# Kernel optimization log

Measured on AMD Instinct MI355X. Metric: run time of the kernel, lower is better.

Reference implementation:

```python
import jax, jax.numpy as jnp
import numpy as np

HIDDEN = 1024
NUM_HEADS = 16
HEAD_DIM = HIDDEN // NUM_HEADS


def setup_inputs() -> dict:
    key = jax.random.key(0)
    ks = jax.random.split(key, 9)
    s = 0.02
    return {
        "x": jax.random.normal(ks[0], (2, 2048, HIDDEN), dtype=jnp.float32),
        "wq": jax.random.normal(ks[1], (HIDDEN, HIDDEN), dtype=jnp.float32) * s,
        "bq": jnp.zeros((HIDDEN,), dtype=jnp.float32),
        "wk": jax.random.normal(ks[2], (HIDDEN, HIDDEN), dtype=jnp.float32) * s,
        "bk": jnp.zeros((HIDDEN,), dtype=jnp.float32),
        "wv": jax.random.normal(ks[3], (HIDDEN, HIDDEN), dtype=jnp.float32) * s,
        "bv": jnp.zeros((HIDDEN,), dtype=jnp.float32),
        "wo": jax.random.normal(ks[4], (HIDDEN, HIDDEN), dtype=jnp.float32) * s,
        "bo": jnp.zeros((HIDDEN,), dtype=jnp.float32),
    }


def reference(x, wq, bq, wk, bk, wv, bv, wo, bo):
    B, S, H = x.shape
    # torch nn.Linear: y = x @ W.T + b
    q = x @ wq.T + bq
    k = x @ wk.T + bk
    v = x @ wv.T + bv
    # [B, S, nH, dH] -> [B, nH, S, dH]
    q = q.reshape(B, S, NUM_HEADS, HEAD_DIM).transpose(0, 2, 1, 3)
    k = k.reshape(B, S, NUM_HEADS, HEAD_DIM).transpose(0, 2, 1, 3)
    v = v.reshape(B, S, NUM_HEADS, HEAD_DIM).transpose(0, 2, 1, 3)
    scores = jnp.einsum("bhqd,bhkd->bhqk", q, k)
    probs = jax.nn.softmax(scores / jnp.sqrt(jnp.float32(HEAD_DIM)), axis=-1)
    context = jnp.einsum("bhqk,bhkd->bhqd", probs, v)
    context = context.transpose(0, 2, 1, 3).reshape(B, S, H)
    return context @ wo.T + bo
```

## Files before the change

### kernel.cpp

```cpp
#include <hip/hip_runtime.h>
#include <hip/hip_bf16.h>
#include <math.h>

#define HID   1024
#define NHEAD 16
#define DHEAD 64
#define BATCH 2
#define SEQ   2048
#define TOK   (BATCH*SEQ)

#define LOG2E_8 0.18033688011112042f

typedef float f32x4  __attribute__((ext_vector_type(4)));
typedef short short8 __attribute__((ext_vector_type(8)));

__device__ __forceinline__ unsigned short f2bf(float f) {
    unsigned int u = __float_as_uint(f);
    u += 0x7FFFu + ((u >> 16) & 1u);
    return (unsigned short)(u >> 16);
}

__device__ __forceinline__ unsigned pk2(float lo, float hi) {
    union { __hip_bfloat162 h; unsigned u; } cv;
    cv.h = __float22bfloat162_rn(make_float2(lo, hi));
    return cv.u;
}

__device__ __forceinline__ float fexp2(float x) {
#if __has_builtin(__builtin_amdgcn_exp2f)
    return __builtin_amdgcn_exp2f(x);
#else
    return __expf(x * 0.6931471805599453f);
#endif
}

__device__ __forceinline__ void gll16(const unsigned short* g, unsigned short* l) {
    __builtin_amdgcn_global_load_lds(
        (const __attribute__((address_space(1))) void*)g,
        (__attribute__((address_space(3))) void*)l, 16, 0, 0);
}

__global__ __launch_bounds__(256) void cvt_bf16(const float* __restrict__ in,
                                                unsigned short* __restrict__ out, int n8) {
    int i = blockIdx.x * 256 + threadIdx.x;
    if (i >= n8) return;
    const float4* p = (const float4*)in;
    float4 a = p[2*i], b = p[2*i+1];
    uint4 r;
    r.x = pk2(a.x, a.y); r.y = pk2(a.z, a.w);
    r.z = pk2(b.x, b.y); r.w = pk2(b.z, b.w);
    ((uint4*)out)[i] = r;
}

__global__ __launch_bounds__(256) void cvt_bf16_w4(
    const float* __restrict__ i0, const float* __restrict__ i1,
    const float* __restrict__ i2, const float* __restrict__ i3,
    unsigned short* __restrict__ o0, unsigned short* __restrict__ o1,
    unsigned short* __restrict__ o2, unsigned short* __restrict__ o3, int n8) {
    int i = blockIdx.x * 256 + threadIdx.x;
    if (i >= n8) return;
    int z = blockIdx.y;
    const float* in = (z==0)?i0:((z==1)?i1:((z==2)?i2:i3));
    unsigned short* out = (z==0)?o0:((z==1)?o1:((z==2)?o2:o3));
    const float s = (z == 0) ? LOG2E_8 : 1.0f;
    const float4* p = (const float4*)in;
    float4 a = p[2*i], b = p[2*i+1];
    uint4 r;
    r.x = pk2(a.x*s, a.y*s); r.y = pk2(a.z*s, a.w*s);
    r.z = pk2(b.x*s, b.y*s); r.w = pk2(b.z*s, b.w*s);
    ((uint4*)out)[i] = r;
}

template<int BM, int BN, int NZ, bool OUTF32, int MINW>
__global__ __launch_bounds__(256, MINW) void gemm_t(
    const unsigned short* __restrict__ A,
    const unsigned short* __restrict__ W0, const unsigned short* __restrict__ W1,
    const unsigned short* __restrict__ W2,
    const float* __restrict__ b0, const float* __restrict__ b1, const float* __restrict__ b2,
    void* __restrict__ C0, void* __restrict__ C1, void* __restrict__ C2,
    int M, int N, int K)
{
    constexpr int MT = BM/32;
    constexpr int NT = BN/32;
    constexpr int AG = BM/64;
    constexpr int WG = BN/64;

    __shared__ unsigned short As[BM*32];
    __shared__ unsigned short Ws[BN*32];

    const unsigned short* W = W0; const float* bias = b0; void* C = C0;
    int z = 0;
    if (NZ > 1) {
        z = blockIdx.z;
        W    = (z==0) ? W0 : ((z==1) ? W1 : W2);
        bias = (z==0) ? b0 : ((z==1) ? b1 : b2);
        C    = (z==0) ? C0 : ((z==1) ? C1 : C2);
    }
    const int tid  = threadIdx.x;
    const int l15  = tid & 15, quad = (tid >> 4) & 3, w = tid >> 6;
    const int wm   = (w >> 1) * (BM/2), wn = (w & 1) * (BN/2);
    const int m0   = blockIdx.y * BM, n0 = blockIdx.x * BN;

    const int lane = tid & 63;
    const int grow = lane >> 2;
    const int gchk = (lane & 3) ^ (grow & 3);

    const unsigned short* pA[AG]; unsigned short* lA[AG];
    const unsigned short* pW[WG]; unsigned short* lW[WG];
    #pragma unroll
    for (int i = 0; i < AG; ++i) {
        const int r = w*(BM/4) + i*16;
        pA[i] = A + (size_t)(m0 + r + grow) * K + gchk*8;
        lA[i] = &As[r * 32];
    }
    #pragma unroll
    for (int i = 0; i < WG; ++i) {
        const int r = w*(BN/4) + i*16;
        pW[i] = W + (size_t)(n0 + r + grow) * K + gchk*8;
        lW[i] = &Ws[r * 32];
    }

    f32x4 acc[MT][NT] = {};

    for (int k0 = 0; k0 < K; k0 += 32) {
        #pragma unroll
        for (int i = 0; i < AG; ++i) { gll16(pA[i], lA[i]); pA[i] += 32; }
        #pragma unroll
        for (int i = 0; i < WG; ++i) { gll16(pW[i], lW[i]); pW[i] += 32; }
        __syncthreads();

        const int co = (quad ^ (l15 & 3)) * 8;
        short8 af[MT], bfv[NT];
        #pragma unroll
        for (int mi = 0; mi < MT; ++mi) af[mi]  = *(const short8*)&As[(wm + mi*16 + l15)*32 + co];
        #pragma unroll
        for (int ni = 0; ni < NT; ++ni) bfv[ni] = *(const short8*)&Ws[(wn + ni*16 + l15)*32 + co];
        #pragma unroll
        for (int mi = 0; mi < MT; ++mi)
            #pragma unroll
            for (int ni = 0; ni < NT; ++ni)
                acc[mi][ni] = __builtin_amdgcn_mfma_f32_16x16x32_bf16(af[mi], bfv[ni], acc[mi][ni], 0, 0, 0);
        __syncthreads();
    }

    const float bsc = (NZ == 3 && z == 0) ? LOG2E_8 : 1.0f;
    float bv[NT];
    #pragma unroll
    for (int ni = 0; ni < NT; ++ni) bv[ni] = bias[n0 + wn + ni*16 + l15] * bsc;

    if (NZ == 3 && z == 2) {
        #pragma unroll
        for (int mi = 0; mi < MT; ++mi)
            #pragma unroll
            for (int ni = 0; ni < NT; ++ni) {
                const int row0 = m0 + wm + mi*16 + quad*4;
                const int col  = n0 + wn + ni*16 + l15;
                const int hh = col >> 6, dd = col & 63;
                const int bb = row0 >> 11, ss = row0 & 2047;
                ushort4 r4;
                r4.x = f2bf(acc[mi][ni][0] + bv[ni]);
                r4.y = f2bf(acc[mi][ni][1] + bv[ni]);
                r4.z = f2bf(acc[mi][ni][2] + bv[ni]);
                r4.w = f2bf(acc[mi][ni][3] + bv[ni]);
                *(ushort4*)((unsigned short*)C + ((size_t)(bb*NHEAD + hh)*DHEAD + dd)*SEQ + ss) = r4;
            }
    } else {
        #pragma unroll
        for (int mi = 0; mi < MT; ++mi)
            #pragma unroll
            for (int ni = 0; ni < NT; ++ni)
                #pragma unroll
                for (int r = 0; r < 4; ++r) {
                    const int row = m0 + wm + mi*16 + quad*4 + r;
                    const int col = n0 + wn + ni*16 + l15;
                    const float val = acc[mi][ni][r] + bv[ni];
                    if (OUTF32) ((float*)C)[(size_t)row*N + col] = val;
                    else ((unsigned short*)C)[(size_t)row*N + col] = f2bf(val);
                }
    }
}

__global__ __launch_bounds__(256, 2) void attn_v5(
    const unsigned short* __restrict__ Qg, const unsigned short* __restrict__ Kg,
    const unsigned short* __restrict__ vT,
    unsigned short* __restrict__ pO0, unsigned short* __restrict__ pO1,
    float* __restrict__ pl)
{
    __shared__ unsigned short Ks[2][64][64];
    __shared__ unsigned short VT[2][64][64];
    __shared__ unsigned short PTs[4*64*64];

    const int tid  = threadIdx.x;
    const int l15  = tid & 15, quad = (tid >> 4) & 3, w = tid >> 6;
    const int z    = blockIdx.z;
    const int b    = z & 1, half = z >> 1;
    const int h    = blockIdx.y;
    const int q0   = blockIdx.x * 256;
    const size_t rowbase = (size_t)b * SEQ;
    const int    cbase   = h * DHEAD;
    const size_t vbase   = (size_t)(b*NHEAD + h) * DHEAD * SEQ;
    const int    keybase = half * (SEQ/2);

    {
        const unsigned short* src = Qg + (rowbase + q0 + tid) * HID + cbase;
        #pragma unroll
        for (int j = 0; j < 8; ++j)
            *(uint4*)&PTs[tid*64 + ((j ^ (tid & 7)) * 8)] = *(const uint4*)(src + j*8);
    }
    short8 qa[4][2];
    #pragma unroll
    for (int nq = 0; nq < 4; ++nq)
        #pragma unroll
        for (int s2 = 0; s2 < 2; ++s2)
            qa[nq][s2] = *(const short8*)&PTs[(w*64 + nq*16 + l15)*64 + (((s2*4 + quad) ^ (l15 & 7)) * 8)];

    const int sr = tid >> 2, sc = (tid & 3) * 16;
    const int c0 = (sc >> 3) ^ (sr & 7);
    const int c1 = ((sc >> 3) + 1) ^ (sr & 7);
    {
        const unsigned short* ks = Kg + (rowbase + keybase + sr) * HID + cbase + sc;
        const unsigned short* vs = vT + vbase + (size_t)sr * SEQ + keybase + sc;
        *(uint4*)&Ks[0][sr][c0*8] = *(const uint4*)ks;
        *(uint4*)&Ks[0][sr][c1*8] = *(const uint4*)(ks + 8);
        *(uint4*)&VT[0][sr][c0*8] = *(const uint4*)vs;
        *(uint4*)&VT[0][sr][c1*8] = *(const uint4*)(vs + 8);
    }

    f32x4 o[4][4] = {};
    float lsum[4] = {0.f, 0.f, 0.f, 0.f};
    unsigned short* myPT = &PTs[w*64*64];

    for (int kt = 0; kt < SEQ/2/64; ++kt) {
        const int buf = kt & 1;
        __syncthreads();

        uint4 kr0, kr1, vr0, vr1;
        const bool pre = (kt + 1 < SEQ/2/64);
        if (pre) {
            const unsigned short* ks = Kg + (rowbase + keybase + (kt+1)*64 + sr) * HID + cbase + sc;
            const unsigned short* vs = vT + vbase + (size_t)sr * SEQ + keybase + (kt+1)*64 + sc;
            kr0 = *(const uint4*)ks; kr1 = *(const uint4*)(ks + 8);
            vr0 = *(const uint4*)vs; vr1 = *(const uint4*)(vs + 8);
        }

        f32x4 s[4][4] = {};
        #pragma unroll
        for (int s2 = 0; s2 < 2; ++s2) {
            short8 kfr[4];
            #pragma unroll
            for (int mi = 0; mi < 4; ++mi)
                kfr[mi] = *(const short8*)&Ks[buf][mi*16 + l15][((s2*4 + quad) ^ (l15 & 7)) * 8];
            #pragma unroll
            for (int mi = 0; mi < 4; ++mi)
                #pragma unroll
                for (int nq = 0; nq < 4; ++nq)
                    s[mi][nq] = __builtin_amdgcn_mfma_f32_16x16x32_bf16(kfr[mi], qa[nq][s2], s[mi][nq], 0, 0, 0);
        }

        #pragma unroll
        for (int mi = 0; mi < 4; ++mi)
            #pragma unroll
            for (int nq = 0; nq < 4; ++nq) {
                const float p0 = fexp2(s[mi][nq][0]);
                const float p1 = fexp2(s[mi][nq][1]);
                const float p2 = fexp2(s[mi][nq][2]);
                const float p3 = fexp2(s[mi][nq][3]);
                lsum[nq] += (p0 + p1) + (p2 + p3);
                uint2 u; u.x = pk2(p0, p1); u.y = pk2(p2, p3);
                const int off = (((2*mi + (quad >> 1)) ^ (l15 & 7)) * 8) + (quad & 1) * 4;
                *(uint2*)&myPT[(nq*16 + l15)*64 + off] = u;
            }

        #pragma unroll
        for (int ks2 = 0; ks2 < 2; ++ks2) {
            short8 ptb[4], vfr[4];
            #pragma unroll
            for (int nq = 0; nq < 4; ++nq)
                ptb[nq] = *(const short8*)&myPT[(nq*16 + l15)*64 + ((ks2*4 + quad) ^ (l15 & 7)) * 8];
            #pragma unroll
            for (int md = 0; md < 4; ++md)
                vfr[md] = *(const short8*)&VT[buf][md*16 + l15][((ks2*4 + quad) ^ (l15 & 7)) * 8];
            #pragma unroll
            for (int md = 0; md < 4; ++md)
                #pragma unroll
                for (int nq = 0; nq < 4; ++nq)
                    o[md][nq] = __builtin_amdgcn_mfma_f32_16x16x32_bf16(vfr[md], ptb[nq], o[md][nq], 0, 0, 0);
        }

        if (pre) {
            const int nb = buf ^ 1;
            *(uint4*)&Ks[nb][sr][c0*8] = kr0;
            *(uint4*)&Ks[nb][sr][c1*8] = kr1;
            *(uint4*)&VT[nb][sr][c0*8] = vr0;
            *(uint4*)&VT[nb][sr][c1*8] = vr1;
        }
    }

    unsigned short* pO = half ? pO1 : pO0;
    #pragma unroll
    for (int nq = 0; nq < 4; ++nq) {
        float l = lsum[nq];
        l += __shfl_xor(l, 16);
        l += __shfl_xor(l, 32);
        if (quad == 0)
            pl[(((size_t)half * BATCH + b) * NHEAD + h) * SEQ + q0 + w*64 + nq*16 + l15] = l;
        const size_t row = rowbase + q0 + w*64 + nq*16 + l15;
        #pragma unroll
        for (int md = 0; md < 4; ++md) {
            ushort4 u;
            u.x = f2bf(o[md][nq][0]); u.y = f2bf(o[md][nq][1]);
            u.z = f2bf(o[md][nq][2]); u.w = f2bf(o[md][nq][3]);
            *(ushort4*)&pO[row * HID + cbase + md*16 + quad*4] = u;
        }
    }
}

__device__ __forceinline__ unsigned addpair(unsigned a, unsigned c, float inv) {
    float a0 = __uint_as_float(a << 16), a1 = __uint_as_float(a & 0xffff0000u);
    float c0 = __uint_as_float(c << 16), c1 = __uint_as_float(c & 0xffff0000u);
    return pk2((a0 + c0) * inv, (a1 + c1) * inv);
}

__global__ __launch_bounds__(256) void reduce_ctx(
    const unsigned short* __restrict__ p0, const unsigned short* __restrict__ p1,
    const float* __restrict__ pl, unsigned short* __restrict__ ctx)
{
    const int i  = blockIdx.x * 256 + threadIdx.x;
    const int e0 = i * 8;
    const int t  = e0 >> 10;
    const int h  = (e0 & 1023) >> 6;
    const int b  = t >> 11, q = t & 2047;
    const float l0 = pl[(((size_t)0 * BATCH + b) * NHEAD + h) * SEQ + q];
    const float l1 = pl[(((size_t)1 * BATCH + b) * NHEAD + h) * SEQ + q];
    const float inv = 1.f / (l0 + l1);
    uint4 a = ((const uint4*)p0)[i];
    uint4 c = ((const uint4*)p1)[i];
    uint4 r;
    r.x = addpair(a.x, c.x, inv);
    r.y = addpair(a.y, c.y, inv);
    r.z = addpair(a.z, c.z, inv);
    r.w = addpair(a.w, c.w, inv);
    ((uint4*)ctx)[i] = r;
}

extern "C" void kernel_launch(void* const* d_in, const int* in_sizes, int n_in,
                              void* d_out, int out_size, void* d_ws, size_t ws_size,
                              hipStream_t stream)
{
    const float* x  = (const float*)d_in[0];
    const float* wq = (const float*)d_in[1];
    const float* bq = (const float*)d_in[2];
    const float* wk = (const float*)d_in[3];
    const float* bk = (const float*)d_in[4];
    const float* wv = (const float*)d_in[5];
    const float* bv = (const float*)d_in[6];
    const float* wo = (const float*)d_in[7];
    const float* bo = (const float*)d_in[8];
    float* out = (float*)d_out;

    unsigned short* xb  = (unsigned short*)d_ws;
    unsigned short* wqb = xb  + (size_t)TOK * HID;
    unsigned short* wkb = wqb + (size_t)HID * HID;
    unsigned short* wvb = wkb + (size_t)HID * HID;
    unsigned short* wob = wvb + (size_t)HID * HID;
    unsigned short* qb  = wob + (size_t)HID * HID;
    unsigned short* kb  = qb  + (size_t)TOK * HID;
    unsigned short* vtb = kb  + (size_t)TOK * HID;
    unsigned short* cb  = vtb + (size_t)TOK * HID;

    const dim3 blk(256);
    cvt_bf16<<<dim3(TOK*HID/8/256), blk, 0, stream>>>(x, xb, TOK*HID/8);
    cvt_bf16_w4<<<dim3(HID*HID/8/256, 4), blk, 0, stream>>>(
        wq, wk, wv, wo, wqb, wkb, wvb, wob, HID*HID/8);

    gemm_t<256, 128, 3, false, 2><<<dim3(HID/128, TOK/256, 3), blk, 0, stream>>>(
        xb, wqb, wkb, wvb, bq, bk, bv, qb, kb, vtb, TOK, HID, HID);

    attn_v5<<<dim3(SEQ/256, NHEAD, 4), blk, 0, stream>>>(
        qb, kb, vtb, cb, xb, (float*)wqb);

    reduce_ctx<<<dim3(TOK*HID/8/256), blk, 0, stream>>>(cb, xb, (float*)wqb, qb);

    gemm_t<128, 64, 1, true, 4><<<dim3(HID/64, TOK/128, 1), blk, 0, stream>>>(
        qb, wob, wob, wob, bo, bo, bo, out, out, out, TOK, HID, HID);
}
```

Measured before the change: 211.2 us.

## Split attention keys four ways with smaller tiles, merge conversions, retile QKV GEMM

Result: faster. 205.3 us (-2.8%).

```diff
diff --git a/kernel.cpp b/kernel.cpp
--- a/kernel.cpp
+++ b/kernel.cpp
@@ -40,29 +40,25 @@
         (__attribute__((address_space(3))) void*)l, 16, 0, 0);
 }
 
-__global__ __launch_bounds__(256) void cvt_bf16(const float* __restrict__ in,
-                                                unsigned short* __restrict__ out, int n8) {
-    int i = blockIdx.x * 256 + threadIdx.x;
-    if (i >= n8) return;
-    const float4* p = (const float4*)in;
-    float4 a = p[2*i], b = p[2*i+1];
-    uint4 r;
-    r.x = pk2(a.x, a.y); r.y = pk2(a.z, a.w);
-    r.z = pk2(b.x, b.y); r.w = pk2(b.z, b.w);
-    ((uint4*)out)[i] = r;
-}
-
-__global__ __launch_bounds__(256) void cvt_bf16_w4(
-    const float* __restrict__ i0, const float* __restrict__ i1,
-    const float* __restrict__ i2, const float* __restrict__ i3,
-    unsigned short* __restrict__ o0, unsigned short* __restrict__ o1,
-    unsigned short* __restrict__ o2, unsigned short* __restrict__ o3, int n8) {
-    int i = blockIdx.x * 256 + threadIdx.x;
-    if (i >= n8) return;
-    int z = blockIdx.y;
-    const float* in = (z==0)?i0:((z==1)?i1:((z==2)?i2:i3));
-    unsigned short* out = (z==0)?o0:((z==1)?o1:((z==2)?o2:o3));
-    const float s = (z == 0) ? LOG2E_8 : 1.0f;
+__global__ __launch_bounds__(256) void cvt_all(
+    const float* __restrict__ x,  const float* __restrict__ wq,
+    const float* __restrict__ wk, const float* __restrict__ wv,
+    const float* __restrict__ wo,
+    unsigned short* __restrict__ xb,  unsigned short* __restrict__ wqb,
+    unsigned short* __restrict__ wkb, unsigned short* __restrict__ wvb,
+    unsigned short* __restrict__ wob, int nx, int nw)
+{
+    const int i = blockIdx.x * 256 + threadIdx.x;
+    const int z = blockIdx.y;
+    const float* in; unsigned short* out; int n; float s = 1.0f;
+    switch (z) {
+        case 0:  in = x;  out = xb;  n = nx; break;
+        case 1:  in = wq; out = wqb; n = nw; s = LOG2E_8; break;
+        case 2:  in = wk; out = wkb; n = nw; break;
+        case 3:  in = wv; out = wvb; n = nw; break;
+        default: in = wo; out = wob; n = nw; break;
+    }
+    if (i >= n) return;
     const float4* p = (const float4*)in;
     float4 a = p[2*i], b = p[2*i+1];
     uint4 r;
@@ -180,15 +176,16 @@
     }
 }
 
-__global__ __launch_bounds__(256, 2) void attn_v5(
+__global__ __launch_bounds__(256, 3) void attn_v6(
     const unsigned short* __restrict__ Qg, const unsigned short* __restrict__ Kg,
     const unsigned short* __restrict__ vT,
     unsigned short* __restrict__ pO0, unsigned short* __restrict__ pO1,
+    unsigned short* __restrict__ pO2, unsigned short* __restrict__ pO3,
     float* __restrict__ pl)
 {
-    __shared__ unsigned short Ks[2][64][64];
-    __shared__ unsigned short VT[2][64][64];
-    __shared__ unsigned short PTs[4*64*64];
+    __shared__ unsigned short Ks[32][64];
+    __shared__ unsigned short VT[64][32];
+    __shared__ unsigned short PT[4][64][32];
 
     const int tid  = threadIdx.x;
     const int l15  = tid & 15, quad = (tid >> 4) & 3, w = tid >> 6;
@@ -199,66 +196,51 @@
     const size_t rowbase = (size_t)b * SEQ;
     const int    cbase   = h * DHEAD;
     const size_t vbase   = (size_t)(b*NHEAD + h) * DHEAD * SEQ;
-    const int    keybase = half * (SEQ/2);
-
-    {
-        const unsigned short* src = Qg + (rowbase + q0 + tid) * HID + cbase;
-        #pragma unroll
-        for (int j = 0; j < 8; ++j)
-            *(uint4*)&PTs[tid*64 + ((j ^ (tid & 7)) * 8)] = *(const uint4*)(src + j*8);
-    }
+    const int    keybase = half * (SEQ/4);
+
     short8 qa[4][2];
     #pragma unroll
     for (int nq = 0; nq < 4; ++nq)
         #pragma unroll
         for (int s2 = 0; s2 < 2; ++s2)
-            qa[nq][s2] = *(const short8*)&PTs[(w*64 + nq*16 + l15)*64 + (((s2*4 + quad) ^ (l15 & 7)) * 8)];
-
-    const int sr = tid >> 2, sc = (tid & 3) * 16;
-    const int c0 = (sc >> 3) ^ (sr & 7);
-    const int c1 = ((sc >> 3) + 1) ^ (sr & 7);
-    {
-        const unsigned short* ks = Kg + (rowbase + keybase + sr) * HID + cbase + sc;
-        const unsigned short* vs = vT + vbase + (size_t)sr * SEQ + keybase + sc;
-        *(uint4*)&Ks[0][sr][c0*8] = *(const uint4*)ks;
-        *(uint4*)&Ks[0][sr][c1*8] = *(const uint4*)(ks + 8);
-        *(uint4*)&VT[0][sr][c0*8] = *(const uint4*)vs;
-        *(uint4*)&VT[0][sr][c1*8] = *(const uint4*)(vs + 8);
-    }
+            qa[nq][s2] = *(const short8*)(Qg + (rowbase + q0 + w*64 + nq*16 + l15) * HID
+                                             + cbase + s2*32 + quad*8);
+
+    const int kr_ = tid >> 3, kc_ = tid & 7;
+    const int ksc = kc_ ^ (kr_ & 7);
+    const int vd_ = tid >> 2, vkc = tid & 3;
+    const int vsc = vkc ^ ((vd_ >> 1) & 3);
+    const unsigned short* kgp = Kg + (rowbase + keybase + kr_) * HID + cbase + kc_*8;
+    const unsigned short* vgp = vT + vbase + (size_t)vd_ * SEQ + keybase + vkc*8;
 
     f32x4 o[4][4] = {};
     float lsum[4] = {0.f, 0.f, 0.f, 0.f};
-    unsigned short* myPT = &PTs[w*64*64];
-
-    for (int kt = 0; kt < SEQ/2/64; ++kt) {
-        const int buf = kt & 1;
+    const int fsw = (l15 >> 1) & 3;
+
+    for (int kt = 0; kt < SEQ/4/32; ++kt) {
+        const uint4 kv4 = *(const uint4*)kgp;  kgp += (size_t)32 * HID;
+        const uint4 vv4 = *(const uint4*)vgp;  vgp += 32;
         __syncthreads();
-
-        uint4 kr0, kr1, vr0, vr1;
-        const bool pre = (kt + 1 < SEQ/2/64);
-        if (pre) {
-            const unsigned short* ks = Kg + (rowbase + keybase + (kt+1)*64 + sr) * HID + cbase + sc;
-            const unsigned short* vs = vT + vbase + (size_t)sr * SEQ + keybase + (kt+1)*64 + sc;
-            kr0 = *(const uint4*)ks; kr1 = *(const uint4*)(ks + 8);
-            vr0 = *(const uint4*)vs; vr1 = *(const uint4*)(vs + 8);
-        }
-
-        f32x4 s[4][4] = {};
+        *(uint4*)&Ks[kr_][ksc*8] = kv4;
+        *(uint4*)&VT[vd_][vsc*8] = vv4;
+        __syncthreads();
+
+        f32x4 s[2][4] = {};
         #pragma unroll
         for (int s2 = 0; s2 < 2; ++s2) {
-            short8 kfr[4];
-            #pragma unroll
-            for (int mi = 0; mi < 4; ++mi)
-                kfr[mi] = *(const short8*)&Ks[buf][mi*16 + l15][((s2*4 + quad) ^ (l15 & 7)) * 8];
-            #pragma unroll
-            for (int mi = 0; mi < 4; ++mi)
+            short8 kf[2];
+            #pragma unroll
+            for (int mi = 0; mi < 2; ++mi)
+                kf[mi] = *(const short8*)&Ks[mi*16 + l15][((((s2<<2)|quad)) ^ (l15 & 7)) * 8];
+            #pragma unroll
+            for (int mi = 0; mi < 2; ++mi)
                 #pragma unroll
                 for (int nq = 0; nq < 4; ++nq)
-                    s[mi][nq] = __builtin_amdgcn_mfma_f32_16x16x32_bf16(kfr[mi], qa[nq][s2], s[mi][nq], 0, 0, 0);
+                    s[mi][nq] = __builtin_amdgcn_mfma_f32_16x16x32_bf16(kf[mi], qa[nq][s2], s[mi][nq], 0, 0, 0);
         }
 
         #pragma unroll
-        for (int mi = 0; mi < 4; ++mi)
+        for (int mi = 0; mi < 2; ++mi)
             #pragma unroll
             for (int nq = 0; nq < 4; ++nq) {
                 const float p0 = fexp2(s[mi][nq][0]);
@@ -267,36 +249,25 @@
                 const float p3 = fexp2(s[mi][nq][3]);
                 lsum[nq] += (p0 + p1) + (p2 + p3);
                 uint2 u; u.x = pk2(p0, p1); u.y = pk2(p2, p3);
-                const int off = (((2*mi + (quad >> 1)) ^ (l15 & 7)) * 8) + (quad & 1) * 4;
-                *(uint2*)&myPT[(nq*16 + l15)*64 + off] = u;
+                const int sc = (2*mi + (quad >> 1)) ^ fsw;
+                *(uint2*)&PT[w][nq*16 + l15][sc*8 + (quad & 1)*4] = u;
             }
 
-        #pragma unroll
-        for (int ks2 = 0; ks2 < 2; ++ks2) {
-            short8 ptb[4], vfr[4];
+        short8 ptb[4], vf[4];
+        #pragma unroll
+        for (int nq = 0; nq < 4; ++nq)
+            ptb[nq] = *(const short8*)&PT[w][nq*16 + l15][(quad ^ fsw) * 8];
+        #pragma unroll
+        for (int md = 0; md < 4; ++md)
+            vf[md] = *(const short8*)&VT[md*16 + l15][(quad ^ fsw) * 8];
+        #pragma unroll
+        for (int md = 0; md < 4; ++md)
             #pragma unroll
             for (int nq = 0; nq < 4; ++nq)
-                ptb[nq] = *(const short8*)&myPT[(nq*16 + l15)*64 + ((ks2*4 + quad) ^ (l15 & 7)) * 8];
-            #pragma unroll
-            for (int md = 0; md < 4; ++md)
-                vfr[md] = *(const short8*)&VT[buf][md*16 + l15][((ks2*4 + quad) ^ (l15 & 7)) * 8];
-            #pragma unroll
-            for (int md = 0; md < 4; ++md)
-                #pragma unroll
-                for (int nq = 0; nq < 4; ++nq)
-                    o[md][nq] = __builtin_amdgcn_mfma_f32_16x16x32_bf16(vfr[md], ptb[nq], o[md][nq], 0, 0, 0);
-        }
-
-        if (pre) {
-            const int nb = buf ^ 1;
-            *(uint4*)&Ks[nb][sr][c0*8] = kr0;
-            *(uint4*)&Ks[nb][sr][c1*8] = kr1;
-            *(uint4*)&VT[nb][sr][c0*8] = vr0;
-            *(uint4*)&VT[nb][sr][c1*8] = vr1;
-        }
-    }
-
-    unsigned short* pO = half ? pO1 : pO0;
+                o[md][nq] = __builtin_amdgcn_mfma_f32_16x16x32_bf16(vf[md], ptb[nq], o[md][nq], 0, 0, 0);
+    }
+
+    unsigned short* pO = (half == 0) ? pO0 : ((half == 1) ? pO1 : ((half == 2) ? pO2 : pO3));
     #pragma unroll
     for (int nq = 0; nq < 4; ++nq) {
         float l = lsum[nq];
@@ -315,14 +286,18 @@
     }
 }
 
-__device__ __forceinline__ unsigned addpair(unsigned a, unsigned c, float inv) {
-    float a0 = __uint_as_float(a << 16), a1 = __uint_as_float(a & 0xffff0000u);
-    float c0 = __uint_as_float(c << 16), c1 = __uint_as_float(c & 0xffff0000u);
-    return pk2((a0 + c0) * inv, (a1 + c1) * inv);
-}
-
-__global__ __launch_bounds__(256) void reduce_ctx(
+__device__ __forceinline__ unsigned addquad(unsigned a, unsigned b, unsigned c,
+                                            unsigned d, float inv) {
+    const float s0 = __uint_as_float(a << 16) + __uint_as_float(b << 16)
+                   + __uint_as_float(c << 16) + __uint_as_float(d << 16);
+    const float s1 = __uint_as_float(a & 0xffff0000u) + __uint_as_float(b & 0xffff0000u)
+                   + __uint_as_float(c & 0xffff0000u) + __uint_as_float(d & 0xffff0000u);
+    return pk2(s0 * inv, s1 * inv);
+}
+
+__global__ __launch_bounds__(256) void reduce4(
     const unsigned short* __restrict__ p0, const unsigned short* __restrict__ p1,
+    const unsigned short* __restrict__ p2, const unsigned short* __restrict__ p3,
     const float* __restrict__ pl, unsigned short* __restrict__ ctx)
 {
     const int i  = blockIdx.x * 256 + threadIdx.x;
@@ -330,16 +305,19 @@
     const int t  = e0 >> 10;
     const int h  = (e0 & 1023) >> 6;
     const int b  = t >> 11, q = t & 2047;
-    const float l0 = pl[(((size_t)0 * BATCH + b) * NHEAD + h) * SEQ + q];
-    const float l1 = pl[(((size_t)1 * BATCH + b) * NHEAD + h) * SEQ + q];
-    const float inv = 1.f / (l0 + l1);
+    const size_t lb = ((size_t)b * NHEAD + h) * SEQ + q;
+    const size_t lstep = (size_t)BATCH * NHEAD * SEQ;
+    const float l = pl[lb] + pl[lb + lstep] + pl[lb + 2*lstep] + pl[lb + 3*lstep];
+    const float inv = 1.f / l;
     uint4 a = ((const uint4*)p0)[i];
-    uint4 c = ((const uint4*)p1)[i];
+    uint4 b4 = ((const uint4*)p1)[i];
+    uint4 c = ((const uint4*)p2)[i];
+    uint4 d = ((const uint4*)p3)[i];
     uint4 r;
-    r.x = addpair(a.x, c.x, inv);
-    r.y = addpair(a.y, c.y, inv);
-    r.z = addpair(a.z, c.z, inv);
-    r.w = addpair(a.w, c.w, inv);
+    r.x = addquad(a.x, b4.x, c.x, d.x, inv);
+    r.y = addquad(a.y, b4.y, c.y, d.y, inv);
+    r.z = addquad(a.z, b4.z, c.z, d.z, inv);
+    r.w = addquad(a.w, b4.w, c.w, d.w, inv);
     ((uint4*)ctx)[i] = r;
 }
 
@@ -367,19 +345,22 @@
     unsigned short* kb  = qb  + (size_t)TOK * HID;
     unsigned short* vtb = kb  + (size_t)TOK * HID;
     unsigned short* cb  = vtb + (size_t)TOK * HID;
+    unsigned short* cb2 = cb  + (size_t)TOK * HID;
+    unsigned short* cb3 = cb2 + (size_t)TOK * HID;
 
     const dim3 blk(256);
-    cvt_bf16<<<dim3(TOK*HID/8/256), blk, 0, stream>>>(x, xb, TOK*HID/8);
-    cvt_bf16_w4<<<dim3(HID*HID/8/256, 4), blk, 0, stream>>>(
-        wq, wk, wv, wo, wqb, wkb, wvb, wob, HID*HID/8);
-
-    gemm_t<256, 128, 3, false, 2><<<dim3(HID/128, TOK/256, 3), blk, 0, stream>>>(
+
+    cvt_all<<<dim3(TOK*HID/8/256, 5), blk, 0, stream>>>(
+        x, wq, wk, wv, wo, xb, wqb, wkb, wvb, wob, TOK*HID/8, HID*HID/8);
+
+    gemm_t<128, 128, 3, false, 3><<<dim3(HID/128, TOK/128, 3), blk, 0, stream>>>(
         xb, wqb, wkb, wvb, bq, bk, bv, qb, kb, vtb, TOK, HID, HID);
 
-    attn_v5<<<dim3(SEQ/256, NHEAD, 4), blk, 0, stream>>>(
-        qb, kb, vtb, cb, xb, (float*)wqb);
-
-    reduce_ctx<<<dim3(TOK*HID/8/256), blk, 0, stream>>>(cb, xb, (float*)wqb, qb);
+    attn_v6<<<dim3(SEQ/256, NHEAD, BATCH*4), blk, 0, stream>>>(
+        qb, kb, vtb, xb, cb, cb2, cb3, (float*)wqb);
+
+    reduce4<<<dim3(TOK*HID/8/256), blk, 0, stream>>>(
+        xb, cb, cb2, cb3, (float*)wqb, qb);
 
     gemm_t<128, 64, 1, true, 4><<<dim3(HID/64, TOK/128, 1), blk, 0, stream>>>(
         qb, wob, wob, wob, bo, bo, bo, out, out, out, TOK, HID, HID);
```
